# Kernel tuning notes

Hardware: AMD Instinct MI355X
Metric: run time of the kernel (lower is better)

## Reference

```python
import jax, jax.numpy as jnp
import numpy as np

B, DIM, H, W = 8, 256, 128, 128
P = 4               # patch_size
HEADS = 8
HD = DIM // HEADS   # head dim = 32
CPB_HIDDEN = 512    # hidden width of the dynamic RPE MLP


def setup_inputs() -> dict:
    key = jax.random.key(0)
    ks = jax.random.split(key, 12)
    s = 0.02
    return {
        "x": jax.random.normal(ks[0], (B, DIM, H, W), dtype=jnp.float32),
        # PatchEmbed2d: Conv2d(dim, dim, kernel=P, stride=P)  weight [O, I, P, P]
        "w_embed": jax.random.normal(ks[1], (DIM, DIM, P, P), dtype=jnp.float32) * s,
        "b_embed": jnp.zeros((DIM,), dtype=jnp.float32),
        # DynamicPosEncoder: MLP(2 -> CPB_HIDDEN -> HEADS) on relative coords
        "cpb_w1": jax.random.normal(ks[2], (CPB_HIDDEN, 2), dtype=jnp.float32) * s,
        "cpb_b1": jnp.zeros((CPB_HIDDEN,), dtype=jnp.float32),
        "cpb_w2": jax.random.normal(ks[3], (HEADS, CPB_HIDDEN), dtype=jnp.float32) * s,
        # MaskAttention2d
        "w_qkv": jax.random.normal(ks[4], (3 * DIM, DIM), dtype=jnp.float32) * s,
        "b_qkv": jnp.zeros((3 * DIM,), dtype=jnp.float32),
        "w_proj": jax.random.normal(ks[5], (DIM, DIM), dtype=jnp.float32) * s,
        "b_proj": jnp.zeros((DIM,), dtype=jnp.float32),
        # PatchUnEmbed2d: ConvTranspose2d(dim, dim, kernel=P, stride=P)  weight [I, O, P, P]
        "w_unembed": jax.random.normal(ks[6], (DIM, DIM, P, P), dtype=jnp.float32) * s,
        "b_unembed": jnp.zeros((DIM,), dtype=jnp.float32),
    }


def _rpe_bias(Hp, Wp, cpb_w1, cpb_b1, cpb_w2):
    """Dynamic relative position bias -> [HEADS, N, N], N = Hp*Wp."""
    # continuous relative-coordinate table [(2Hp-1)*(2Wp-1), 2], normalized to [-1, 1]
    rh = (jnp.arange(2 * Hp - 1, dtype=jnp.float32) - (Hp - 1)) / max(Hp - 1, 1)
    rw = (jnp.arange(2 * Wp - 1, dtype=jnp.float32) - (Wp - 1)) / max(Wp - 1, 1)
    rel = jnp.stack(jnp.meshgrid(rh, rw, indexing="ij"), axis=-1).reshape(-1, 2)
    table = jax.nn.relu(rel @ cpb_w1.T + cpb_b1) @ cpb_w2.T  # [(2Hp-1)(2Wp-1), HEADS]
    # static relative position index [N, N]
    ch = np.arange(Hp)
    cw = np.arange(Wp)
    coords = np.stack(np.meshgrid(ch, cw, indexing="ij")).reshape(2, -1)  # [2, N]
    d = coords[:, :, None] - coords[:, None, :]                           # [2, N, N]
    idx = (d[0] + Hp - 1) * (2 * Wp - 1) + (d[1] + Wp - 1)               # [N, N]
    bias = table[jnp.asarray(idx)]                                        # [N, N, HEADS]
    return bias.transpose(2, 0, 1)                                        # [HEADS, N, N]


def reference(x, w_embed, b_embed, cpb_w1, cpb_b1, cpb_w2,
              w_qkv, b_qkv, w_proj, b_proj, w_unembed, b_unembed):
    Bx, C, Hf, Wf = x.shape
    Hp, Wp = Hf // P, Wf // P
    N = Hp * Wp
    # ---- patch embed: Conv2d(k=P, s=P) as block reshape + einsum ----
    xr = x.reshape(Bx, C, Hp, P, Wp, P)
    z = jnp.einsum("bchpwq,ocpq->bohw", xr, w_embed) + b_embed[None, :, None, None]
    # ---- dynamic RPE bias ----
    bias = _rpe_bias(Hp, Wp, cpb_w1, cpb_b1, cpb_w2)  # [HEADS, N, N]
    # ---- multi-head self-attention over the Hp*Wp grid ----
    tok = z.reshape(Bx, C, N).transpose(0, 2, 1)                     # [B, N, C]
    qkv = tok @ w_qkv.T + b_qkv                                       # [B, N, 3C]
    qkv = qkv.reshape(Bx, N, 3, HEADS, HD).transpose(2, 0, 3, 1, 4)   # [3, B, H, N, hd]
    q, k, v = qkv[0], qkv[1], qkv[2]
    scale = HD ** -0.5
    attn = jnp.einsum("bhnd,bhmd->bhnm", q * scale, k) + bias[None]   # [B, H, N, N]
    attn = jax.nn.softmax(attn, axis=-1)
    out = jnp.einsum("bhnm,bhmd->bhnd", attn, v)                      # [B, H, N, hd]
    out = out.transpose(0, 2, 1, 3).reshape(Bx, N, C)
    out = out @ w_proj.T + b_proj                                     # [B, N, C]
    z2 = out.transpose(0, 2, 1).reshape(Bx, C, Hp, Wp)
    # ---- patch unembed: ConvTranspose2d(k=P, s=P) as einsum + block reshape ----
    y = jnp.einsum("bchw,copq->bohpwq", z2, w_unembed)
    y = y.reshape(Bx, C, Hf, Wf) + b_unembed[None, :, None, None]
    return y
```

## Files before the change

kernel.cpp:

```cpp
#include <hip/hip_runtime.h>
#include <cstdint>
#include <cstddef>


typedef __bf16 bf16x8 __attribute__((ext_vector_type(8)));
typedef float f32x4 __attribute__((ext_vector_type(4)));
typedef unsigned short u16x4 __attribute__((ext_vector_type(4)));

__device__ __forceinline__ unsigned short f2bf(float f) {
  unsigned u = __builtin_bit_cast(unsigned, f);
  u += 0x7fffu + ((u >> 16) & 1u);
  return (unsigned short)(u >> 16);
}
__device__ __forceinline__ float bf2f(unsigned short u) {
  return __builtin_bit_cast(float, ((unsigned)u) << 16);
}

__device__ __forceinline__ void async_ld16(const void* g, void* l) {
  __builtin_amdgcn_global_load_lds(
      (const __attribute__((address_space(1))) void*)g,
      (__attribute__((address_space(3))) void*)l, 16, 0, 0);
}

__device__ __forceinline__ void cvt8_store(unsigned short* dst, float4 a,
                                           float4 b) {
  unsigned short t[8] = {f2bf(a.x), f2bf(a.y), f2bf(a.z), f2bf(a.w),
                         f2bf(b.x), f2bf(b.y), f2bf(b.z), f2bf(b.w)};
  *(uint4*)dst = *(const uint4*)t;
}

__global__ __launch_bounds__(256) void rpe_table_kernel(
    const float* __restrict__ w1, const float* __restrict__ b1,
    const float* __restrict__ w2, float* __restrict__ tableT) {
  int t = blockIdx.x * 256 + threadIdx.x;
  if (t >= 3969) return;
  int a = t / 63, c = t - a * 63;
  float rh = (float)(a - 31) * (1.0f / 31.0f);
  float rw = (float)(c - 31) * (1.0f / 31.0f);
  float acc[8];
#pragma unroll
  for (int h = 0; h < 8; h++) acc[h] = 0.f;
  for (int j = 0; j < 512; j++) {
    float hv = fmaxf(rh * w1[2 * j] + rw * w1[2 * j + 1] + b1[j], 0.f);
#pragma unroll
    for (int h = 0; h < 8; h++) acc[h] += hv * w2[h * 512 + j];
  }
#pragma unroll
  for (int h = 0; h < 8; h++) tableT[h * 4096 + t] = acc[h];
}

__global__ __launch_bounds__(256) void cvt_bf16_kernel(
    const float* __restrict__ src, unsigned short* __restrict__ dst, int n8) {
  int i = blockIdx.x * 256 + threadIdx.x;
  if (i >= n8) return;
  const float4* s4 = (const float4*)src + (size_t)i * 2;
  float4 a = s4[0], b = s4[1];
  unsigned short t[8] = {f2bf(a.x), f2bf(a.y), f2bf(a.z), f2bf(a.w),
                         f2bf(b.x), f2bf(b.y), f2bf(b.z), f2bf(b.w)};
  *(uint4*)(dst + (size_t)i * 8) = *(const uint4*)t;
}

__global__ __launch_bounds__(256) void transpose_cvt_kernel(
    const float* __restrict__ src, unsigned short* __restrict__ dst) {
  __shared__ float tile[32][33];
  int bx = blockIdx.x;
  int by = blockIdx.y;
  int tx = threadIdx.x & 31, ty = threadIdx.x >> 5;
#pragma unroll
  for (int r = 0; r < 32; r += 8)
    tile[ty + r][tx] = src[(size_t)(by * 32 + ty + r) * 4096 + bx * 32 + tx];
  __syncthreads();
#pragma unroll
  for (int r = 0; r < 32; r += 8)
    dst[(size_t)(bx * 32 + ty + r) * 256 + by * 32 + tx] = f2bf(tile[tx][ty + r]);
}

template <int NS>
__global__ __launch_bounds__(256) void splitk_reduce_kernel(
    const float* __restrict__ part, const float* __restrict__ bias,
    unsigned short* __restrict__ out) {
  size_t i = ((size_t)blockIdx.x * 256 + threadIdx.x) * 8;
  const float4* p = (const float4*)(part + i);
  const size_t s4 = 2097152 / 4;
  float4 a0 = p[0], a1 = p[1];
#pragma unroll
  for (int s = 1; s < NS; s++) {
    float4 b0 = p[s * s4], b1 = p[s * s4 + 1];
    a0.x += b0.x; a0.y += b0.y; a0.z += b0.z; a0.w += b0.w;
    a1.x += b1.x; a1.y += b1.y; a1.z += b1.z; a1.w += b1.w;
  }
  int col = (int)(i & 255);
  unsigned short t8[8] = {
      f2bf(a0.x + bias[col + 0]), f2bf(a0.y + bias[col + 1]),
      f2bf(a0.z + bias[col + 2]), f2bf(a0.w + bias[col + 3]),
      f2bf(a1.x + bias[col + 4]), f2bf(a1.y + bias[col + 5]),
      f2bf(a1.z + bias[col + 6]), f2bf(a1.w + bias[col + 7])};
  *(uint4*)(out + i) = *(const uint4*)t8;
}

__global__ __launch_bounds__(256) void gemm_embed_kernel(
    const float* __restrict__ x, const unsigned short* __restrict__ Bw,
    float* __restrict__ Cpart) {
  __shared__ unsigned short As[2 * 128 * 32];
  __shared__ unsigned short Bs[2 * 128 * 32];
  int tid = threadIdx.x;
  int lane = tid & 63, wave = tid >> 6;

  int L = blockIdx.x;
  int xcd = L & 7, j = L >> 3;
  int pair = xcd * 64 + (j >> 1);
  int n0 = (j & 1) * 128;
  int z = pair & 7, y = pair >> 3;
  int m0 = y * 128;
  int wm = (wave & 1) * 64, wn = (wave >> 1) * 64;
  int fr = lane & 15, fh = lane >> 4;

  f32x4 acc[4][4];
#pragma unroll
  for (int i = 0; i < 4; i++)
#pragma unroll
    for (int jj = 0; jj < 4; jj++) acc[i][jj] = (f32x4){0.f, 0.f, 0.f, 0.f};

  int f0 = tid, f1 = tid + 256;
  const unsigned short* Bg0 =
      Bw + (size_t)(n0 + (f0 >> 2)) * 4096 + z * 512 + (f0 & 3) * 8;
  const unsigned short* Bg1 =
      Bw + (size_t)(n0 + (f1 >> 2)) * 4096 + z * 512 + (f1 & 3) * 8;
  unsigned short* Bl0 = Bs + f0 * 8;
  unsigned short* Bl1 = Bs + f1 * 8;

  const float4* x4 = (const float4*)x;
  int r0 = f0 >> 2, ch0 = f0 & 3;
  int m_0 = m0 + r0, b_0 = m_0 >> 10, hp0 = (m_0 >> 5) & 31, wp0 = m_0 & 31;
  int c_0 = z * 32 + (ch0 >> 1), p_0 = (2 * ch0) & 3;
  const float4* xp0 =
      x4 + (size_t)((b_0 * 256 + c_0) * 128 + hp0 * 4 + p_0) * 32 + wp0;
  int r1 = f1 >> 2, ch1 = f1 & 3;
  int m_1 = m0 + r1, b_1 = m_1 >> 10, hp1 = (m_1 >> 5) & 31, wp1 = m_1 & 31;
  int c_1 = z * 32 + (ch1 >> 1), p_1 = (2 * ch1) & 3;
  const float4* xp1 =
      x4 + (size_t)((b_1 * 256 + c_1) * 128 + hp1 * 4 + p_1) * 32 + wp1;
  unsigned short* Al0 = As + f0 * 8;
  unsigned short* Al1 = As + f1 * 8;

  float4 a00 = xp0[0], a01 = xp0[32], a10 = xp1[0], a11 = xp1[32];
  xp0 += 8192; xp1 += 8192;
  async_ld16(Bg0, Bl0);
  async_ld16(Bg1, Bl1);
  cvt8_store(Al0, a00, a01);
  cvt8_store(Al1, a10, a11);
  __syncthreads();

  for (int t = 0; t < 16; t++) {
    int cur = (t & 1) << 12, nxt = cur ^ 4096;
    if (t < 15) {
      a00 = xp0[0]; a01 = xp0[32]; a10 = xp1[0]; a11 = xp1[32];
      xp0 += 8192; xp1 += 8192;
      int kn = (t + 1) << 5;
      async_ld16(Bg0 + kn, Bl0 + nxt);
      async_ld16(Bg1 + kn, Bl1 + nxt);
    }
    const unsigned short* Asc = As + cur;
    const unsigned short* Bsc = Bs + cur;
    bf16x8 af[4], bfr[4];
#pragma unroll
    for (int tt = 0; tt < 4; tt++) {
      af[tt] = *(const bf16x8*)(Asc + (wm + tt * 16 + fr) * 32 + fh * 8);
      bfr[tt] = *(const bf16x8*)(Bsc + (wn + tt * 16 + fr) * 32 + fh * 8);
    }
#pragma unroll
    for (int mt = 0; mt < 4; mt++)
#pragma unroll
      for (int nt = 0; nt < 4; nt++)
        acc[mt][nt] = __builtin_amdgcn_mfma_f32_16x16x32_bf16(
            af[mt], bfr[nt], acc[mt][nt], 0, 0, 0);
    if (t < 15) {
      cvt8_store(Al0 + nxt, a00, a01);
      cvt8_store(Al1 + nxt, a10, a11);
    }
    __syncthreads();
  }

  float* Cp = Cpart + (size_t)z * 2097152;
#pragma unroll
  for (int mt = 0; mt < 4; mt++) {
    int row0 = m0 + wm + mt * 16 + fh * 4;
#pragma unroll
    for (int nt = 0; nt < 4; nt++) {
      int col = n0 + wn + nt * 16 + fr;
#pragma unroll
      for (int r = 0; r < 4; r++)
        Cp[(size_t)(row0 + r) * 256 + col] = acc[mt][nt][r];
    }
  }
}

template <int CMODE>
__global__ __launch_bounds__(256) void gemm_mfma_kernel(
    const unsigned short* __restrict__ A, const unsigned short* __restrict__ B,
    const float* __restrict__ bias, void* __restrict__ Cv,
    int M, int N, int K, int lda, int ldb, int ldc) {
  __shared__ unsigned short As[2 * 128 * 32];
  __shared__ unsigned short Bs[2 * 128 * 32];
  int tid = threadIdx.x;
  int lane = tid & 63;
  int wave = tid >> 6;
  int m0 = blockIdx.y * 128, n0 = blockIdx.x * 128;
  int wm = (wave & 1) * 64, wn = (wave >> 1) * 64;

  if (CMODE == 4) {
    int s = blockIdx.z;
    A += (size_t)s * K;
    B += (size_t)s * K;
    Cv = (void*)((float*)Cv + (size_t)s * M * N);
  }

  f32x4 acc[4][4];
#pragma unroll
  for (int i = 0; i < 4; i++)
#pragma unroll
    for (int j = 0; j < 4; j++) acc[i][j] = (f32x4){0.f, 0.f, 0.f, 0.f};

  int f0 = tid, f1 = tid + 256;
  const unsigned short* Ag0 = A + (size_t)(m0 + (f0 >> 2)) * lda + (f0 & 3) * 8;
  const unsigned short* Ag1 = A + (size_t)(m0 + (f1 >> 2)) * lda + (f1 & 3) * 8;
  const unsigned short* Bg0 = B + (size_t)(n0 + (f0 >> 2)) * ldb + (f0 & 3) * 8;
  const unsigned short* Bg1 = B + (size_t)(n0 + (f1 >> 2)) * ldb + (f1 & 3) * 8;
  unsigned short* Al0 = As + f0 * 8;
  unsigned short* Al1 = As + f1 * 8;
  unsigned short* Bl0 = Bs + f0 * 8;
  unsigned short* Bl1 = Bs + f1 * 8;

  int fr = lane & 15;
  int fh = lane >> 4;

  int ntiles = K >> 5;
  async_ld16(Ag0, Al0);
  async_ld16(Ag1, Al1);
  async_ld16(Bg0, Bl0);
  async_ld16(Bg1, Bl1);
  __syncthreads();

  for (int t = 0; t < ntiles; t++) {
    int cur = (t & 1) << 12;
    int nxt = cur ^ 4096;
    if (t + 1 < ntiles) {
      int kn = (t + 1) << 5;
      async_ld16(Ag0 + kn, Al0 + nxt);
      async_ld16(Ag1 + kn, Al1 + nxt);
      async_ld16(Bg0 + kn, Bl0 + nxt);
      async_ld16(Bg1 + kn, Bl1 + nxt);
    }
    const unsigned short* Asc = As + cur;
    const unsigned short* Bsc = Bs + cur;
    bf16x8 af[4], bfr[4];
#pragma unroll
    for (int tt = 0; tt < 4; tt++) {
      af[tt] = *(const bf16x8*)(Asc + (wm + tt * 16 + fr) * 32 + fh * 8);
      bfr[tt] = *(const bf16x8*)(Bsc + (wn + tt * 16 + fr) * 32 + fh * 8);
    }
#pragma unroll
    for (int mt = 0; mt < 4; mt++)
#pragma unroll
      for (int nt = 0; nt < 4; nt++)
        acc[mt][nt] = __builtin_amdgcn_mfma_f32_16x16x32_bf16(
            af[mt], bfr[nt], acc[mt][nt], 0, 0, 0);
    __syncthreads();
  }

#pragma unroll
  for (int mt = 0; mt < 4; mt++) {
    int row0 = m0 + wm + mt * 16 + fh * 4;
    if (CMODE == 2) {
      int b = row0 >> 10, hp = (row0 >> 5) & 31, wp = row0 & 31;
      size_t rowoff0 = (size_t)b * 4194304 + hp * 512 + wp * 4;
      float* y = (float*)Cv;
#pragma unroll
      for (int nt = 0; nt < 4; nt++) {
        int col = n0 + wn + nt * 16 + fr;
        int o = col >> 4, p = (col >> 2) & 3, q = col & 3;
        size_t coloff = (size_t)o * 16384 + p * 128 + q;
        float bv = bias[o];
#pragma unroll
        for (int r = 0; r < 4; r++)
          y[rowoff0 + r * 4 + coloff] = acc[mt][nt][r] + bv;
      }
    } else if (CMODE == 3) {
      unsigned short* base = (unsigned short*)Cv;
#pragma unroll
      for (int nt = 0; nt < 4; nt++) {
        int col = n0 + wn + nt * 16 + fr;
        int which = col >> 8, hh = (col >> 5) & 7, d = col & 31;
        float bv = bias[col];
#pragma unroll
        for (int r = 0; r < 4; r++) {
          int row = row0 + r;
          int bb = row >> 10, nn = row & 1023;
          int bh = bb * 8 + hh;
          float v = acc[mt][nt][r] + bv;
          if (which == 0) v *= 0.17677669529663687f;
          size_t addr;
          if (which < 2)
            addr = (size_t)which * 2097152 + ((size_t)bh * 1024 + nn) * 32 + d;
          else
            addr = (size_t)2 * 2097152 + (size_t)bh * 32768 + (size_t)d * 1024 + nn;
          base[addr] = f2bf(v);
        }
      }
    } else if (CMODE == 4) {
      float* Cp = (float*)Cv;
#pragma unroll
      for (int nt = 0; nt < 4; nt++) {
        int col = n0 + wn + nt * 16 + fr;
#pragma unroll
        for (int r = 0; r < 4; r++)
          Cp[(size_t)(row0 + r) * ldc + col] = acc[mt][nt][r];
      }
    } else {
#pragma unroll
      for (int nt = 0; nt < 4; nt++) {
        int col = n0 + wn + nt * 16 + fr;
        float bv = bias ? bias[col] : 0.f;
        unsigned short* C = (unsigned short*)Cv;
#pragma unroll
        for (int r = 0; r < 4; r++)
          C[(size_t)(row0 + r) * ldc + col] = f2bf(acc[mt][nt][r] + bv);
      }
    }
  }
}

__global__ __launch_bounds__(512) void attn_mfma_kernel(
    const unsigned short* __restrict__ Qb, const unsigned short* __restrict__ Kb,
    const unsigned short* __restrict__ Vtb,
    const float* __restrict__ tableT,
    unsigned short* __restrict__ out) {
  __shared__ float th[3972];
  __shared__ unsigned short Ps[2][8][1088];

  int tid = threadIdx.x;
  int lane = tid & 63, w = tid >> 6;
  int n = lane & 15, g = lane >> 4;
  int blk = blockIdx.x;
  int h = blk & 7, b = (blk >> 3) & 7, qt = blk >> 6;
  int bh = b * 8 + h;
  int q0 = qt * 128;

  const unsigned short* Qg = Qb + ((size_t)bh * 1024 + q0) * 32;
  const unsigned short* Kg = Kb + (size_t)bh * 1024 * 32;
  const unsigned short* Vg = Vtb + (size_t)bh * 32 * 1024;
  const float* tg = tableT + (size_t)h * 4096;

  for (int i = tid; i < 3969; i += 512) th[i] = tg[i];
  bf16x8 qf = *(const bf16x8*)(Qg + (size_t)(w * 16 + n) * 32 + g * 8);
  __syncthreads();

  f32x4 oacc[2];
  oacc[0] = (f32x4){0.f, 0.f, 0.f, 0.f};
  oacc[1] = (f32x4){0.f, 0.f, 0.f, 0.f};
  float m_run = -1e30f, l_run = 0.f;

  int q = q0 + w * 16 + n;
  int tbase = (q >> 5) * 63 + (q & 31) + 1984;

  unsigned short* PwA = &Ps[0][w][0];
  unsigned short* PwB = &Ps[1][w][0];

  bf16x8 kfA[4], kfB[4];
#pragma unroll
  for (int mt = 0; mt < 4; mt++)
    kfA[mt] = *(const bf16x8*)(Kg + (size_t)(mt * 16 + n) * 32 + g * 8);

  auto half_step = [&](const bf16x8 (&kf)[4], int k0, unsigned short* Pw) {
    bf16x8 vf[4];
#pragma unroll
    for (int i = 0; i < 4; i++)
      vf[i] = *(const bf16x8*)(Vg + (size_t)((i & 1) * 16 + n) * 1024 + k0 +
                               (i >> 1) * 32 + g * 8);

    f32x4 s[4];
    __builtin_amdgcn_s_setprio(1);
#pragma unroll
    for (int mt = 0; mt < 4; mt++)
      s[mt] = __builtin_amdgcn_mfma_f32_16x16x32_bf16(
          kf[mt], qf, (f32x4){0.f, 0.f, 0.f, 0.f}, 0, 0, 0);
    __builtin_amdgcn_s_setprio(0);

#pragma unroll
    for (int mt = 0; mt < 4; mt++) {
      int kb = k0 + mt * 16 + g * 4;
      int ib = tbase - (kb >> 5) * 63 - (kb & 31);
      s[mt][0] += th[ib];
      s[mt][1] += th[ib - 1];
      s[mt][2] += th[ib - 2];
      s[mt][3] += th[ib - 3];
    }

    float mx = -1e30f;
#pragma unroll
    for (int mt = 0; mt < 4; mt++)
#pragma unroll
      for (int r = 0; r < 4; r++) mx = fmaxf(mx, s[mt][r]);
    mx = fmaxf(mx, __shfl_xor(mx, 16, 64));
    mx = fmaxf(mx, __shfl_xor(mx, 32, 64));
    float m_new = fmaxf(m_run, mx);
    float alpha = __expf(m_run - m_new);
    m_run = m_new;

    float ls = 0.f;
#pragma unroll
    for (int mt = 0; mt < 4; mt++) {
#pragma unroll
      for (int r = 0; r < 4; r++) {
        float p = __expf(s[mt][r] - m_new);
        s[mt][r] = p;
        ls += p;
      }
      u16x4 pk = {f2bf(s[mt][0]), f2bf(s[mt][1]), f2bf(s[mt][2]),
                  f2bf(s[mt][3])};
      *(u16x4*)(Pw + n * 68 + mt * 16 + g * 4) = pk;
    }
    l_run = l_run * alpha + ls;

#pragma unroll
    for (int dt = 0; dt < 2; dt++)
#pragma unroll
      for (int r = 0; r < 4; r++) oacc[dt][r] *= alpha;
    __builtin_amdgcn_s_setprio(1);
#pragma unroll
    for (int kt = 0; kt < 2; kt++) {
      bf16x8 pf = *(const bf16x8*)(Pw + n * 68 + kt * 32 + g * 8);
      oacc[0] = __builtin_amdgcn_mfma_f32_16x16x32_bf16(vf[kt * 2 + 0], pf,
                                                        oacc[0], 0, 0, 0);
      oacc[1] = __builtin_amdgcn_mfma_f32_16x16x32_bf16(vf[kt * 2 + 1], pf,
                                                        oacc[1], 0, 0, 0);
    }
    __builtin_amdgcn_s_setprio(0);
  };

  for (int tt = 0; tt < 8; tt++) {
    int k0 = tt * 128;
#pragma unroll
    for (int mt = 0; mt < 4; mt++)
      kfB[mt] = *(const bf16x8*)(Kg + (size_t)(k0 + 64 + mt * 16 + n) * 32 +
                                 g * 8);
    half_step(kfA, k0, PwA);
    if (tt < 7) {
#pragma unroll
      for (int mt = 0; mt < 4; mt++)
        kfA[mt] = *(const bf16x8*)(Kg + (size_t)(k0 + 128 + mt * 16 + n) * 32 +
                                   g * 8);
    }
    half_step(kfB, k0 + 64, PwB);
  }

  float l = l_run;
  l += __shfl_xor(l, 16, 64);
  l += __shfl_xor(l, 32, 64);
  float invl = 1.f / l;
  unsigned short* ob = out + ((size_t)(b * 1024 + q) * 256) + h * 32;
#pragma unroll
  for (int dt = 0; dt < 2; dt++) {
    u16x4 o4 = {f2bf(oacc[dt][0] * invl), f2bf(oacc[dt][1] * invl),
                f2bf(oacc[dt][2] * invl), f2bf(oacc[dt][3] * invl)};
    *(u16x4*)(ob + dt * 16 + g * 4) = o4;
  }
}

extern "C" void kernel_launch(void* const* d_in, const int* in_sizes, int n_in,
                              void* d_out, int out_size, void* d_ws, size_t ws_size,
                              hipStream_t stream) {
  const float* x         = (const float*)d_in[0];
  const float* w_embed   = (const float*)d_in[1];
  const float* b_embed   = (const float*)d_in[2];
  const float* cpb_w1    = (const float*)d_in[3];
  const float* cpb_b1    = (const float*)d_in[4];
  const float* cpb_w2    = (const float*)d_in[5];
  const float* w_qkv     = (const float*)d_in[6];
  const float* b_qkv     = (const float*)d_in[7];
  const float* w_proj    = (const float*)d_in[8];
  const float* b_proj    = (const float*)d_in[9];
  const float* w_unembed = (const float*)d_in[10];
  const float* b_unembed = (const float*)d_in[11];
  float* out = (float*)d_out;

  char* w = (char*)d_ws;
  float*          ProjP = (float*)w;          w += (size_t)8388608 * 4;
  unsigned short* tok   = (unsigned short*)w; w += (size_t)8192 * 256 * 2;
  unsigned short* wE    = (unsigned short*)w; w += (size_t)1048576 * 2;
  unsigned short* wQ    = (unsigned short*)w; w += (size_t)196608 * 2;
  unsigned short* wP    = (unsigned short*)w; w += (size_t)65536 * 2;
  unsigned short* wUt   = (unsigned short*)w; w += (size_t)1048576 * 2;
  float*          tableT= (float*)w;          w += (size_t)32768 * 4;
  float*          PART  = (float*)w;          w += (size_t)8 * 2097152 * 4;

  unsigned short* qkvB  = (unsigned short*)PART;
  unsigned short* attno = (unsigned short*)((char*)PART + 12582912);
  unsigned short* z2    = (unsigned short*)((char*)PART + 16777216);
  unsigned short* Qb  = qkvB;
  unsigned short* Kb  = qkvB + 2097152;
  unsigned short* Vtb = qkvB + 2 * 2097152;

  cvt_bf16_kernel<<<512, 256, 0, stream>>>(w_embed, wE, 131072);
  cvt_bf16_kernel<<<96, 256, 0, stream>>>(w_qkv, wQ, 24576);
  cvt_bf16_kernel<<<32, 256, 0, stream>>>(w_proj, wP, 8192);
  transpose_cvt_kernel<<<dim3(128, 8), 256, 0, stream>>>(w_unembed, wUt);
  rpe_table_kernel<<<16, 256, 0, stream>>>(cpb_w1, cpb_b1, cpb_w2, tableT);

  gemm_embed_kernel<<<1024, 256, 0, stream>>>(x, wE, PART);
  splitk_reduce_kernel<8><<<1024, 256, 0, stream>>>(PART, b_embed, tok);

  gemm_mfma_kernel<3><<<dim3(6, 64), 256, 0, stream>>>(
      tok, wQ, b_qkv, qkvB, 8192, 768, 256, 256, 256, 0);

  attn_mfma_kernel<<<512, 512, 0, stream>>>(Qb, Kb, Vtb, tableT, attno);

  gemm_mfma_kernel<4><<<dim3(2, 64, 4), 256, 0, stream>>>(
      attno, wP, nullptr, ProjP, 8192, 256, 64, 256, 256, 256);
  splitk_reduce_kernel<4><<<1024, 256, 0, stream>>>(ProjP, b_proj, z2);

  gemm_mfma_kernel<2><<<dim3(32, 64), 256, 0, stream>>>(
      z2, wUt, b_unembed, out, 8192, 4096, 256, 256, 256, 0);
}
```

Before: 507.7 us.

## Halve embed split-K and deepen its load pipeline with raw waitcnt barriers

The patch-embed GEMM drops from 8-way to 4-way split-K, so each block runs 32 K-steps and the partial buffer and reduce pass shrink by half. Its main loop is now software-pipelined two steps ahead: a 4-stage B buffer filled by async LDS loads, register double-buffering for the activation loads, and explicit s_waitcnt/s_barrier in place of __syncthreads. MFMA sections are wrapped in s_setprio. The grid halves to 512 blocks, which lowers parallelism, and the hand-counted vmcnt values must match the number of outstanding loads or correctness breaks.

```diff
diff --git a/kernel.cpp b/kernel.cpp
--- a/kernel.cpp
+++ b/kernel.cpp
@@ -101,16 +101,16 @@
 __global__ __launch_bounds__(256) void gemm_embed_kernel(
     const float* __restrict__ x, const unsigned short* __restrict__ Bw,
     float* __restrict__ Cpart) {
-  __shared__ unsigned short As[2 * 128 * 32];
-  __shared__ unsigned short Bs[2 * 128 * 32];
+  __shared__ unsigned short As[2 * 4096];
+  __shared__ unsigned short Bs[4 * 4096];
   int tid = threadIdx.x;
   int lane = tid & 63, wave = tid >> 6;
 
   int L = blockIdx.x;
   int xcd = L & 7, j = L >> 3;
-  int pair = xcd * 64 + (j >> 1);
+  int pair = xcd * 32 + (j >> 1);
   int n0 = (j & 1) * 128;
-  int z = pair & 7, y = pair >> 3;
+  int z = pair & 3, y = pair >> 2;
   int m0 = y * 128;
   int wm = (wave & 1) * 64, wn = (wave >> 1) * 64;
   int fr = lane & 15, fh = lane >> 4;
@@ -123,62 +123,70 @@
 
   int f0 = tid, f1 = tid + 256;
   const unsigned short* Bg0 =
-      Bw + (size_t)(n0 + (f0 >> 2)) * 4096 + z * 512 + (f0 & 3) * 8;
+      Bw + (size_t)(n0 + (f0 >> 2)) * 4096 + z * 1024 + (f0 & 3) * 8;
   const unsigned short* Bg1 =
-      Bw + (size_t)(n0 + (f1 >> 2)) * 4096 + z * 512 + (f1 & 3) * 8;
+      Bw + (size_t)(n0 + (f1 >> 2)) * 4096 + z * 1024 + (f1 & 3) * 8;
   unsigned short* Bl0 = Bs + f0 * 8;
   unsigned short* Bl1 = Bs + f1 * 8;
 
   const float4* x4 = (const float4*)x;
   int r0 = f0 >> 2, ch0 = f0 & 3;
   int m_0 = m0 + r0, b_0 = m_0 >> 10, hp0 = (m_0 >> 5) & 31, wp0 = m_0 & 31;
-  int c_0 = z * 32 + (ch0 >> 1), p_0 = (2 * ch0) & 3;
+  int c_0 = z * 64 + (ch0 >> 1), p_0 = (2 * ch0) & 3;
   const float4* xp0 =
       x4 + (size_t)((b_0 * 256 + c_0) * 128 + hp0 * 4 + p_0) * 32 + wp0;
   int r1 = f1 >> 2, ch1 = f1 & 3;
   int m_1 = m0 + r1, b_1 = m_1 >> 10, hp1 = (m_1 >> 5) & 31, wp1 = m_1 & 31;
-  int c_1 = z * 32 + (ch1 >> 1), p_1 = (2 * ch1) & 3;
+  int c_1 = z * 64 + (ch1 >> 1), p_1 = (2 * ch1) & 3;
   const float4* xp1 =
       x4 + (size_t)((b_1 * 256 + c_1) * 128 + hp1 * 4 + p_1) * 32 + wp1;
   unsigned short* Al0 = As + f0 * 8;
   unsigned short* Al1 = As + f1 * 8;
 
-  float4 a00 = xp0[0], a01 = xp0[32], a10 = xp1[0], a11 = xp1[32];
-  xp0 += 8192; xp1 += 8192;
+  float4 aP[4], aQ[4];
+
+  aP[0] = xp0[0]; aP[1] = xp0[32]; aP[2] = xp1[0]; aP[3] = xp1[32];
   async_ld16(Bg0, Bl0);
   async_ld16(Bg1, Bl1);
-  cvt8_store(Al0, a00, a01);
-  cvt8_store(Al1, a10, a11);
-  __syncthreads();
-
-  for (int t = 0; t < 16; t++) {
-    int cur = (t & 1) << 12, nxt = cur ^ 4096;
-    if (t < 15) {
-      a00 = xp0[0]; a01 = xp0[32]; a10 = xp1[0]; a11 = xp1[32];
-      xp0 += 8192; xp1 += 8192;
-      int kn = (t + 1) << 5;
-      async_ld16(Bg0 + kn, Bl0 + nxt);
-      async_ld16(Bg1 + kn, Bl1 + nxt);
-    }
-    const unsigned short* Asc = As + cur;
-    const unsigned short* Bsc = Bs + cur;
+  asm volatile("" ::: "memory");
+  aQ[0] = xp0[8192]; aQ[1] = xp0[8224]; aQ[2] = xp1[8192]; aQ[3] = xp1[8224];
+  async_ld16(Bg0 + 32, Bl0 + 4096);
+  async_ld16(Bg1 + 32, Bl1 + 4096);
+  cvt8_store(Al0, aP[0], aP[1]);
+  cvt8_store(Al1, aP[2], aP[3]);
+  asm volatile("s_waitcnt vmcnt(6) lgkmcnt(0)\n\ts_barrier" ::: "memory");
+
+  auto half = [&](int t, float4 (&aCur)[4], float4 (&aNext)[4]) {
+    const unsigned short* Asc = As + ((t & 1) << 12);
+    const unsigned short* Bsc = Bs + ((t & 3) << 12);
     bf16x8 af[4], bfr[4];
 #pragma unroll
     for (int tt = 0; tt < 4; tt++) {
       af[tt] = *(const bf16x8*)(Asc + (wm + tt * 16 + fr) * 32 + fh * 8);
       bfr[tt] = *(const bf16x8*)(Bsc + (wn + tt * 16 + fr) * 32 + fh * 8);
     }
+    int tc = (t + 2 > 31) ? 31 : t + 2;
+    size_t ax = (size_t)tc * 8192;
+    aCur[0] = xp0[ax]; aCur[1] = xp0[ax + 32];
+    aCur[2] = xp1[ax]; aCur[3] = xp1[ax + 32];
+    async_ld16(Bg0 + (tc << 5), Bl0 + ((tc & 3) << 12));
+    async_ld16(Bg1 + (tc << 5), Bl1 + ((tc & 3) << 12));
+    __builtin_amdgcn_s_setprio(1);
 #pragma unroll
     for (int mt = 0; mt < 4; mt++)
 #pragma unroll
       for (int nt = 0; nt < 4; nt++)
         acc[mt][nt] = __builtin_amdgcn_mfma_f32_16x16x32_bf16(
             af[mt], bfr[nt], acc[mt][nt], 0, 0, 0);
-    if (t < 15) {
-      cvt8_store(Al0 + nxt, a00, a01);
-      cvt8_store(Al1 + nxt, a10, a11);
-    }
-    __syncthreads();
+    __builtin_amdgcn_s_setprio(0);
+    cvt8_store(Al0 + (((t + 1) & 1) << 12), aNext[0], aNext[1]);
+    cvt8_store(Al1 + (((t + 1) & 1) << 12), aNext[2], aNext[3]);
+    asm volatile("s_waitcnt vmcnt(6) lgkmcnt(0)\n\ts_barrier" ::: "memory");
+  };
+
+  for (int it = 0; it < 16; it++) {
+    half(2 * it, aP, aQ);
+    half(2 * it + 1, aQ, aP);
   }
 
   float* Cp = Cpart + (size_t)z * 2097152;
@@ -492,7 +500,7 @@
   unsigned short* wP    = (unsigned short*)w; w += (size_t)65536 * 2;
   unsigned short* wUt   = (unsigned short*)w; w += (size_t)1048576 * 2;
   float*          tableT= (float*)w;          w += (size_t)32768 * 4;
-  float*          PART  = (float*)w;          w += (size_t)8 * 2097152 * 4;
+  float*          PART  = (float*)w;          w += (size_t)4 * 2097152 * 4;
 
   unsigned short* qkvB  = (unsigned short*)PART;
   unsigned short* attno = (unsigned short*)((char*)PART + 12582912);
@@ -507,8 +515,8 @@
   transpose_cvt_kernel<<<dim3(128, 8), 256, 0, stream>>>(w_unembed, wUt);
   rpe_table_kernel<<<16, 256, 0, stream>>>(cpb_w1, cpb_b1, cpb_w2, tableT);
 
-  gemm_embed_kernel<<<1024, 256, 0, stream>>>(x, wE, PART);
-  splitk_reduce_kernel<8><<<1024, 256, 0, stream>>>(PART, b_embed, tok);
+  gemm_embed_kernel<<<512, 256, 0, stream>>>(x, wE, PART);
+  splitk_reduce_kernel<4><<<1024, 256, 0, stream>>>(PART, b_embed, tok);
 
   gemm_mfma_kernel<3><<<dim3(6, 64), 256, 0, stream>>>(
       tok, wQ, b_qkv, qkvB, 8192, 768, 256, 256, 256, 0);
```

Measured after the change: 483.2 us. 4.8% less time.
